# Optimization experiments

Hardware: AMD Instinct MI355X
Metric: run time of the kernel (lower is better)

The kernel has to match this reference:

```python
import jax, jax.numpy as jnp
import numpy as np

NEG_SLOPE = 0.01  # torch nn.LeakyReLU default
N_NODES = 100000
N_EDGES = 500000
IN_DIM, OUT_DIM, EF_DIM, EMB_DIM = 128, 128, 64, 256


def leaky_relu(x):
    return jnp.where(x >= 0, x, NEG_SLOPE * x)


def setup_inputs() -> dict:
    key = jax.random.key(0)
    ks = jax.random.split(key, 8)
    s = 0.05
    nf = jax.random.normal(ks[0], (N_NODES, IN_DIM), dtype=jnp.float32)
    ef = jax.random.normal(ks[1], (N_EDGES, EF_DIM), dtype=jnp.float32)
    src = jax.random.randint(ks[2], (N_EDGES,), 0, N_NODES, dtype=jnp.int32)
    dst = jax.random.randint(ks[3], (N_EDGES,), 0, N_NODES, dtype=jnp.int32)
    # Linear weights stored as (in, out); y = x @ W. No biases (bias=False).
    We1 = jax.random.normal(ks[4], (2 * IN_DIM + EF_DIM, EMB_DIM), dtype=jnp.float32) * s
    We2 = jax.random.normal(ks[5], (EMB_DIM, OUT_DIM), dtype=jnp.float32) * s
    Wn1 = jax.random.normal(ks[6], (IN_DIM + OUT_DIM, EMB_DIM), dtype=jnp.float32) * s
    Wn2 = jax.random.normal(ks[7], (EMB_DIM, OUT_DIM), dtype=jnp.float32) * s
    return {"nf": nf, "ef": ef, "src": src, "dst": dst,
            "We1": We1, "We2": We2, "Wn1": Wn1, "Wn2": Wn2}


def reference(nf, ef, src, dst, We1, We2, Wn1, Wn2):
    # Symmetrize: add reversed edges carrying the same edge features.
    src_full = jnp.concatenate([src, dst])            # [2E]
    dst_full = jnp.concatenate([dst, src])            # [2E]
    ef_full = jnp.concatenate([ef, ef], axis=0)       # [2E, ef_dim]

    # message_func: MLP over [src_nf | dst_nf | ef]
    edge_in = jnp.concatenate([nf[src_full], nf[dst_full], ef_full], axis=-1)  # [2E, 2*in+ef]
    msg = leaky_relu(edge_in @ We1) @ We2              # [2E, out]

    # reduce_func: sum messages per destination node (zeros for isolated nodes)
    red = jax.ops.segment_sum(msg, dst_full, num_segments=nf.shape[0])  # [N, out]

    # apply_node_func: MLP over [nf | red_msg]
    node_in = jnp.concatenate([nf, red], axis=-1)      # [N, in+out]
    out_nf = leaky_relu(node_in @ Wn1) @ Wn2           # [N, out]
    return out_nf
```

## Files before the change

kernel.cpp:

```cpp
#include <hip/hip_runtime.h>
#include <hip/hip_bf16.h>
#include <string.h>


using f32x4  = __attribute__((ext_vector_type(4))) float;
using bf16x8 = __attribute__((ext_vector_type(8))) short;

#define P128 132
#define P256 264
#define YROW 132

__device__ __forceinline__ float lrelu(float x) { return x >= 0.f ? x : 0.01f * x; }

__device__ __forceinline__ ushort f2bf(float f) {
    union { float f; unsigned u; } v; v.f = f;
    unsigned u = v.u;
    return (ushort)((u + 0x7fffu + ((u >> 16) & 1u)) >> 16);
}
__device__ __forceinline__ float bf2f(ushort u) {
    union { unsigned u; float f; } v; v.u = ((unsigned)u) << 16; return v.f;
}

__device__ __forceinline__ void atomic_pk_add_bf16(void* addr, unsigned val) {
    asm volatile("global_atomic_pk_add_bf16 %0, %1, off" : : "v"(addr), "v"(val) : "memory");
}

__global__ __launch_bounds__(256) void gemm_ab(
    const ushort* __restrict__ X,
    const ushort* __restrict__ Wt,
    ushort* __restrict__ out)
{
    __shared__ ushort Xs[128 * P128];
    const int tid  = threadIdx.x;
    const int lane = tid & 63;
    const int wv   = tid >> 6;
    const int wm   = wv >> 1, wn = wv & 1;
    const int row0 = blockIdx.x * 128;

    #pragma unroll
    for (int q = 0; q < 8; ++q) {
        int idx = q * 256 + tid;
        int r = idx >> 4, c = idx & 15;
        *reinterpret_cast<uint4*>(&Xs[r * P128 + c * 8]) =
            *reinterpret_cast<const uint4*>(X + (size_t)(row0 + r) * 128 + c * 8);
    }
    __syncthreads();

    const int g8 = (lane >> 4) * 8;
    for (int cb = 0; cb < 4; ++cb) {
        f32x4 acc[4][4] = {};
        #pragma unroll
        for (int ks = 0; ks < 4; ++ks) {
            bf16x8 af[4], bf[4];
            #pragma unroll
            for (int i = 0; i < 4; ++i) {
                int mrow = wm * 64 + i * 16 + (lane & 15);
                af[i] = *reinterpret_cast<const bf16x8*>(&Xs[mrow * P128 + ks * 32 + g8]);
                int nc = cb * 128 + wn * 64 + i * 16 + (lane & 15);
                bf[i] = *reinterpret_cast<const bf16x8*>(Wt + (size_t)nc * 128 + ks * 32 + g8);
            }
            #pragma unroll
            for (int i = 0; i < 4; ++i)
                #pragma unroll
                for (int j = 0; j < 4; ++j)
                    acc[i][j] = __builtin_amdgcn_mfma_f32_16x16x32_bf16(af[i], bf[j], acc[i][j], 0, 0, 0);
        }
        #pragma unroll
        for (int i = 0; i < 4; ++i) {
            int gr0 = row0 + wm * 64 + i * 16 + ((lane >> 4) << 2);
            #pragma unroll
            for (int j = 0; j < 4; ++j) {
                int gc = cb * 128 + wn * 64 + j * 16 + (lane & 15);
                #pragma unroll
                for (int r = 0; r < 4; ++r)
                    out[(size_t)(gr0 + r) * 512 + gc] = f2bf(acc[i][j][r]);
            }
        }
    }
}

__global__ __launch_bounds__(256) void edge_msg(
    const ushort* __restrict__ efb,
    const ushort* __restrict__ Wet,
    const ushort* __restrict__ We2t,
    const ushort* __restrict__ AB,
    const int* __restrict__ src, const int* __restrict__ dst,
    ushort* __restrict__ H,
    int E)
{
    __shared__ ushort Ms[64 * P256];
    __shared__ ushort Cs[32 * P256];
    __shared__ int own_s[64], oth_s[64];

    const int tid  = threadIdx.x;
    const int lane = tid & 63;
    const int wv   = tid >> 6;
    const int eb   = blockIdx.x * 32;
    const int g8   = (lane >> 4) * 8;

    if (tid < 32) {
        int e = eb + tid;
        int s_ = (e < E) ? src[e] : -1;
        int d_ = (e < E) ? dst[e] : -1;
        own_s[tid]      = d_;
        oth_s[tid]      = (s_ < 0) ? 0 : s_;
        own_s[32 + tid] = s_;
        oth_s[32 + tid] = (d_ < 0) ? 0 : d_;
    }

    f32x4 ac[2][4] = {};
    #pragma unroll
    for (int ks = 0; ks < 2; ++ks) {
        bf16x8 af[2], bf[4];
        #pragma unroll
        for (int i = 0; i < 2; ++i) {
            int er = i * 16 + (lane & 15);
            af[i] = *reinterpret_cast<const bf16x8*>(efb + (size_t)(eb + er) * 64 + ks * 32 + g8);
        }
        #pragma unroll
        for (int j = 0; j < 4; ++j) {
            int nc = wv * 64 + j * 16 + (lane & 15);
            bf[j] = *reinterpret_cast<const bf16x8*>(Wet + (size_t)nc * 64 + ks * 32 + g8);
        }
        #pragma unroll
        for (int i = 0; i < 2; ++i)
            #pragma unroll
            for (int j = 0; j < 4; ++j)
                ac[i][j] = __builtin_amdgcn_mfma_f32_16x16x32_bf16(af[i], bf[j], ac[i][j], 0, 0, 0);
    }
    #pragma unroll
    for (int i = 0; i < 2; ++i) {
        int er0 = i * 16 + ((lane >> 4) << 2);
        #pragma unroll
        for (int j = 0; j < 4; ++j) {
            int fc = wv * 64 + j * 16 + (lane & 15);
            #pragma unroll
            for (int r = 0; r < 4; ++r)
                Cs[(er0 + r) * P256 + fc] = f2bf(ac[i][j][r]);
        }
    }
    __syncthreads();

    #pragma unroll 4
    for (int p = 0; p < 16; ++p) {
        int m   = p * 4 + wv;
        int oth = oth_s[m];
        int own = own_s[m];
        int ownc = (own < 0) ? 0 : own;
        int rc  = m & 31;
        #pragma unroll
        for (int h = 0; h < 2; ++h) {
            int c = h * 128 + lane * 2;
            ushort2 av = *(const ushort2*)(AB + (size_t)oth  * 512 + c);
            ushort2 bv = *(const ushort2*)(AB + (size_t)ownc * 512 + 256 + c);
            ushort2 cv = *(const ushort2*)(&Cs[rc * P256 + c]);
            ushort2 mv;
            mv.x = f2bf(lrelu(bf2f(av.x) + bf2f(bv.x) + bf2f(cv.x)));
            mv.y = f2bf(lrelu(bf2f(av.y) + bf2f(bv.y) + bf2f(cv.y)));
            *(ushort2*)(&Ms[m * P256 + c]) = mv;
        }
    }
    __syncthreads();

    const int wm = wv >> 1, wn = wv & 1;
    f32x4 ay[2][4] = {};
    #pragma unroll
    for (int ks = 0; ks < 8; ++ks) {
        bf16x8 af[2], bf[4];
        #pragma unroll
        for (int i = 0; i < 2; ++i) {
            int mrow = wm * 32 + i * 16 + (lane & 15);
            af[i] = *reinterpret_cast<const bf16x8*>(&Ms[mrow * P256 + ks * 32 + g8]);
        }
        #pragma unroll
        for (int j = 0; j < 4; ++j) {
            int nc = wn * 64 + j * 16 + (lane & 15);
            bf[j] = *reinterpret_cast<const bf16x8*>(We2t + (size_t)nc * 256 + ks * 32 + g8);
        }
        #pragma unroll
        for (int i = 0; i < 2; ++i)
            #pragma unroll
            for (int j = 0; j < 4; ++j)
                ay[i][j] = __builtin_amdgcn_mfma_f32_16x16x32_bf16(af[i], bf[j], ay[i][j], 0, 0, 0);
    }
    ushort* Ys = Cs;
    #pragma unroll
    for (int i = 0; i < 2; ++i) {
        int yr0 = wm * 32 + i * 16 + ((lane >> 4) << 2);
        #pragma unroll
        for (int j = 0; j < 4; ++j) {
            int yc = wn * 64 + j * 16 + (lane & 15);
            #pragma unroll
            for (int r = 0; r < 4; ++r)
                Ys[(yr0 + r) * YROW + yc] = f2bf(ay[i][j][r]);
        }
    }
    __syncthreads();

    #pragma unroll 4
    for (int q = 0; q < 16; ++q) {
        int row  = wv * 16 + q;
        int node = own_s[row];
        if (node < 0) continue;
        ushort2 yv = *(const ushort2*)(&Ys[row * YROW + lane * 2]);
        unsigned uv; memcpy(&uv, &yv, 4);
        atomic_pk_add_bf16(H + (size_t)node * 128 + lane * 2, uv);
    }
}

__global__ __launch_bounds__(256) void mlp_fused(
    const ushort* __restrict__ H,
    const ushort* __restrict__ nfb,
    const ushort* __restrict__ Wn1t,
    const ushort* __restrict__ Wn2t,
    float* __restrict__ out, int Nreal)
{
    __shared__ ushort lds[128 * P256];
    ushort* Ns  = lds;
    ushort* Rs  = lds + 128 * P128;
    ushort* Hid = lds;

    const int tid  = threadIdx.x;
    const int lane = tid & 63;
    const int wv   = tid >> 6;
    const int wm   = wv >> 1, wn = wv & 1;
    const int row0 = blockIdx.x * 128;
    const int g8   = (lane >> 4) * 8;

    #pragma unroll
    for (int q = 0; q < 8; ++q) {
        int idx = q * 256 + tid;
        int r = idx >> 4, c = (idx & 15) * 8;
        *reinterpret_cast<uint4*>(&Ns[r * P128 + c]) =
            *reinterpret_cast<const uint4*>(nfb + (size_t)(row0 + r) * 128 + c);
        *reinterpret_cast<uint4*>(&Rs[r * P128 + c]) =
            *reinterpret_cast<const uint4*>(H + (size_t)(row0 + r) * 128 + c);
    }
    __syncthreads();

    f32x4 a2[2][4][4] = {};
    #pragma unroll
    for (int cb = 0; cb < 2; ++cb) {
        #pragma unroll
        for (int ks = 0; ks < 8; ++ks) {
            bf16x8 af[4], bf[4];
            #pragma unroll
            for (int i = 0; i < 4; ++i) {
                int mrow = wm * 64 + i * 16 + (lane & 15);
                af[i] = (ks < 4)
                    ? *reinterpret_cast<const bf16x8*>(&Ns[mrow * P128 + ks * 32 + g8])
                    : *reinterpret_cast<const bf16x8*>(&Rs[mrow * P128 + (ks - 4) * 32 + g8]);
                int nc = cb * 128 + wn * 64 + i * 16 + (lane & 15);
                bf[i] = *reinterpret_cast<const bf16x8*>(Wn1t + (size_t)nc * 256 + ks * 32 + g8);
            }
            #pragma unroll
            for (int i = 0; i < 4; ++i)
                #pragma unroll
                for (int j = 0; j < 4; ++j)
                    a2[cb][i][j] = __builtin_amdgcn_mfma_f32_16x16x32_bf16(af[i], bf[j], a2[cb][i][j], 0, 0, 0);
        }
    }
    __syncthreads();

    #pragma unroll
    for (int cb = 0; cb < 2; ++cb)
        #pragma unroll
        for (int i = 0; i < 4; ++i) {
            int er0 = wm * 64 + i * 16 + ((lane >> 4) << 2);
            #pragma unroll
            for (int j = 0; j < 4; ++j) {
                int fc = cb * 128 + wn * 64 + j * 16 + (lane & 15);
                #pragma unroll
                for (int r = 0; r < 4; ++r)
                    Hid[(er0 + r) * P256 + fc] = f2bf(lrelu(a2[cb][i][j][r]));
            }
        }
    __syncthreads();

    f32x4 a3[4][4] = {};
    #pragma unroll
    for (int ks = 0; ks < 8; ++ks) {
        bf16x8 af[4], bf[4];
        #pragma unroll
        for (int i = 0; i < 4; ++i) {
            int mrow = wm * 64 + i * 16 + (lane & 15);
            af[i] = *reinterpret_cast<const bf16x8*>(&Hid[mrow * P256 + ks * 32 + g8]);
            int nc = wn * 64 + i * 16 + (lane & 15);
            bf[i] = *reinterpret_cast<const bf16x8*>(Wn2t + (size_t)nc * 256 + ks * 32 + g8);
        }
        #pragma unroll
        for (int i = 0; i < 4; ++i)
            #pragma unroll
            for (int j = 0; j < 4; ++j)
                a3[i][j] = __builtin_amdgcn_mfma_f32_16x16x32_bf16(af[i], bf[j], a3[i][j], 0, 0, 0);
    }
    #pragma unroll
    for (int i = 0; i < 4; ++i) {
        int gr0 = row0 + wm * 64 + i * 16 + ((lane >> 4) << 2);
        #pragma unroll
        for (int j = 0; j < 4; ++j) {
            int gc = wn * 64 + j * 16 + (lane & 15);
            #pragma unroll
            for (int r = 0; r < 4; ++r) {
                int gr = gr0 + r;
                if (gr < Nreal) out[(size_t)gr * 128 + gc] = a3[i][j][r];
            }
        }
    }
}

__global__ __launch_bounds__(256) void cvt_pad(
    const float* __restrict__ x, ushort* __restrict__ y, size_t n_real, size_t n_pad)
{
    size_t i = ((size_t)blockIdx.x * 256 + threadIdx.x) * 4;
    if (i >= n_pad) return;
    ushort4 o;
    if (i < n_real) {
        float4 v = *(const float4*)(x + i);
        o.x = f2bf(v.x); o.y = f2bf(v.y); o.z = f2bf(v.z); o.w = f2bf(v.w);
    } else { o.x = 0; o.y = 0; o.z = 0; o.w = 0; }
    *(ushort4*)(y + i) = o;
}

__global__ __launch_bounds__(256) void wcvt(
    const float* __restrict__ We1, const float* __restrict__ We2,
    const float* __restrict__ Wn1, const float* __restrict__ Wn2,
    ushort* __restrict__ Wabt, ushort* __restrict__ Wet, ushort* __restrict__ We2t,
    ushort* __restrict__ Wn1t, ushort* __restrict__ Wn2t)
{
    int idx = blockIdx.x * 256 + threadIdx.x;
    switch (blockIdx.y) {
    case 0: if (idx < 256*128) { int n = idx >> 7, k = idx & 127; Wabt[idx]            = f2bf(We1[k * 256 + n]); } break;
    case 1: if (idx < 256*128) { int n = idx >> 7, k = idx & 127; Wabt[32768 + idx]    = f2bf(We1[(128 + k) * 256 + n]); } break;
    case 2: if (idx < 256*64)  { int n = idx >> 6, k = idx & 63;  Wet[idx]             = f2bf(We1[(256 + k) * 256 + n]); } break;
    case 3: if (idx < 128*256) { int n = idx >> 8, k = idx & 255; We2t[idx]            = f2bf(We2[k * 128 + n]); } break;
    case 4: if (idx < 256*256) { int n = idx >> 8, k = idx & 255; Wn1t[idx]            = f2bf(Wn1[k * 256 + n]); } break;
    case 5: if (idx < 128*256) { int n = idx >> 8, k = idx & 255; Wn2t[idx]            = f2bf(Wn2[k * 128 + n]); } break;
    }
}

extern "C" void kernel_launch(void* const* d_in, const int* in_sizes, int n_in,
                              void* d_out, int out_size, void* d_ws, size_t ws_size,
                              hipStream_t stream) {
    const float* nf  = (const float*)d_in[0];
    const float* ef  = (const float*)d_in[1];
    const int*   src = (const int*)d_in[2];
    const int*   dst = (const int*)d_in[3];
    const float* We1 = (const float*)d_in[4];
    const float* We2 = (const float*)d_in[5];
    const float* Wn1 = (const float*)d_in[6];
    const float* Wn2 = (const float*)d_in[7];
    float* out = (float*)d_out;

    const int  N  = in_sizes[0] / 128;
    const int  E  = in_sizes[2];
    const int  Np = (N + 127) & ~127;
    const long Ep = ((long)E + 127) & ~127L;

    char* p = (char*)d_ws;
    auto alloc = [&](size_t bytes) { char* r = p; p += (bytes + 255) & ~(size_t)255; return r; };
    ushort* AB   = (ushort*)alloc((size_t)Np * 512 * 2);
    ushort* H    = (ushort*)alloc((size_t)Np * 128 * 2);
    ushort* nfb  = (ushort*)alloc((size_t)Np * 128 * 2);
    ushort* efb  = (ushort*)alloc((size_t)Ep * 64 * 2);
    ushort* Wabt = (ushort*)alloc(65536 * 2);
    ushort* Wet  = (ushort*)alloc(16384 * 2);
    ushort* We2t = (ushort*)alloc(32768 * 2);
    ushort* Wn1t = (ushort*)alloc(65536 * 2);
    ushort* Wn2t = (ushort*)alloc(32768 * 2);

    dim3 blk(256);

    wcvt<<<dim3(256, 6), blk, 0, stream>>>(We1, We2, Wn1, Wn2, Wabt, Wet, We2t, Wn1t, Wn2t);
    cvt_pad<<<dim3((unsigned)((size_t)Np * 128 / 1024)), blk, 0, stream>>>(nf, nfb, (size_t)N * 128, (size_t)Np * 128);
    cvt_pad<<<dim3((unsigned)((size_t)Ep * 64 / 1024)), blk, 0, stream>>>(ef, efb, (size_t)E * 64, (size_t)Ep * 64);

    gemm_ab<<<dim3(Np / 128), blk, 0, stream>>>(nfb, Wabt, AB);

    hipMemsetAsync(H, 0, (size_t)Np * 128 * 2, stream);

    edge_msg<<<dim3((unsigned)(Ep / 32)), blk, 0, stream>>>(
        efb, Wet, We2t, AB, src, dst, H, E);

    mlp_fused<<<dim3(Np / 128), blk, 0, stream>>>(H, nfb, Wn1t, Wn2t, out, N);
}
```

Before: 771.5 us.

## Sort directed edges by destination and pre-reduce messages before atomic adds

Adds a counting sort (count, single-block scan, scatter) that groups the 2E directed edge records by owning destination node. The edge kernel now processes 64 sorted records per block, gathers edge features by index, prefetches gathered AB rows in registers across phases, and sums consecutive messages for the same node locally before one bf16 atomic per run. The aim is fewer global atomics and better locality on the destination side. In exchange it adds several launches, a serial single-block scan over 100k nodes, atomic scatter ordering, and an indirect edge-feature gather.

```diff
diff --git a/kernel.cpp b/kernel.cpp
--- a/kernel.cpp
+++ b/kernel.cpp
@@ -9,6 +9,7 @@
 #define P128 132
 #define P256 264
 #define YROW 132
+#define VPB  64
 
 __device__ __forceinline__ float lrelu(float x) { return x >= 0.f ? x : 0.01f * x; }
 
@@ -79,84 +80,169 @@
     }
 }
 
-__global__ __launch_bounds__(256) void edge_msg(
+__global__ __launch_bounds__(256) void ebin_count(
+    const int* __restrict__ src, const int* __restrict__ dst,
+    int* __restrict__ cnt, int E)
+{
+    int i = blockIdx.x * 256 + threadIdx.x;
+    if (i >= E) return;
+    atomicAdd(&cnt[dst[i]], 1);
+    atomicAdd(&cnt[src[i]], 1);
+}
+
+__global__ __launch_bounds__(256) void escan(
+    const int* __restrict__ cnt, int* __restrict__ cur, int n)
+{
+    __shared__ int ps[256];
+    const int t = threadIdx.x;
+    const int per = (n + 255) / 256;
+    int s = 0;
+    for (int i = 0; i < per; ++i) { int idx = t * per + i; if (idx < n) s += cnt[idx]; }
+    ps[t] = s;
+    __syncthreads();
+    for (int off = 1; off < 256; off <<= 1) {
+        int u = (t >= off) ? ps[t - off] : 0;
+        __syncthreads();
+        ps[t] += u;
+        __syncthreads();
+    }
+    int run = ps[t] - s;
+    for (int i = 0; i < per; ++i) {
+        int idx = t * per + i;
+        if (idx < n) { cur[idx] = run; run += cnt[idx]; }
+    }
+}
+
+__global__ __launch_bounds__(256) void escatter(
+    const int* __restrict__ src, const int* __restrict__ dst,
+    int* __restrict__ cur, int4* __restrict__ vrec, int E)
+{
+    int i = blockIdx.x * 256 + threadIdx.x;
+    if (i >= E) return;
+    int s_ = src[i], d_ = dst[i];
+    int p1 = atomicAdd(&cur[d_], 1);
+    vrec[p1] = make_int4(d_, s_, i, 0);
+    int p2 = atomicAdd(&cur[s_], 1);
+    vrec[p2] = make_int4(s_, d_, i, 0);
+}
+
+__global__ __launch_bounds__(256) void edge_sorted(
     const ushort* __restrict__ efb,
     const ushort* __restrict__ Wet,
     const ushort* __restrict__ We2t,
     const ushort* __restrict__ AB,
-    const int* __restrict__ src, const int* __restrict__ dst,
+    const int4* __restrict__ vrec,
     ushort* __restrict__ H,
-    int E)
-{
-    __shared__ ushort Ms[64 * P256];
-    __shared__ ushort Cs[32 * P256];
-    __shared__ int own_s[64], oth_s[64];
+    int NV)
+{
+    __shared__ ushort Ms[VPB * P256];
+    __shared__ ushort efs[VPB * 72];
+    __shared__ int so[VPB], st_[VPB], se[VPB];
 
     const int tid  = threadIdx.x;
     const int lane = tid & 63;
     const int wv   = tid >> 6;
-    const int eb   = blockIdx.x * 32;
     const int g8   = (lane >> 4) * 8;
-
-    if (tid < 32) {
-        int e = eb + tid;
-        int s_ = (e < E) ? src[e] : -1;
-        int d_ = (e < E) ? dst[e] : -1;
-        own_s[tid]      = d_;
-        oth_s[tid]      = (s_ < 0) ? 0 : s_;
-        own_s[32 + tid] = s_;
-        oth_s[32 + tid] = (d_ < 0) ? 0 : d_;
-    }
-
-    f32x4 ac[2][4] = {};
-    #pragma unroll
-    for (int ks = 0; ks < 2; ++ks) {
-        bf16x8 af[2], bf[4];
-        #pragma unroll
-        for (int i = 0; i < 2; ++i) {
-            int er = i * 16 + (lane & 15);
-            af[i] = *reinterpret_cast<const bf16x8*>(efb + (size_t)(eb + er) * 64 + ks * 32 + g8);
-        }
-        #pragma unroll
-        for (int j = 0; j < 4; ++j) {
-            int nc = wv * 64 + j * 16 + (lane & 15);
-            bf[j] = *reinterpret_cast<const bf16x8*>(Wet + (size_t)nc * 64 + ks * 32 + g8);
-        }
-        #pragma unroll
-        for (int i = 0; i < 2; ++i)
-            #pragma unroll
-            for (int j = 0; j < 4; ++j)
-                ac[i][j] = __builtin_amdgcn_mfma_f32_16x16x32_bf16(af[i], bf[j], ac[i][j], 0, 0, 0);
-    }
-    #pragma unroll
-    for (int i = 0; i < 2; ++i) {
-        int er0 = i * 16 + ((lane >> 4) << 2);
-        #pragma unroll
-        for (int j = 0; j < 4; ++j) {
-            int fc = wv * 64 + j * 16 + (lane & 15);
-            #pragma unroll
-            for (int r = 0; r < 4; ++r)
-                Cs[(er0 + r) * P256 + fc] = f2bf(ac[i][j][r]);
-        }
-    }
-    __syncthreads();
-
-    #pragma unroll 4
-    for (int p = 0; p < 16; ++p) {
-        int m   = p * 4 + wv;
-        int oth = oth_s[m];
-        int own = own_s[m];
-        int ownc = (own < 0) ? 0 : own;
-        int rc  = m & 31;
+    const int v0   = blockIdx.x * VPB;
+
+    if (tid < VPB) {
+        int v = v0 + tid;
+        if (v < NV) { int4 r = vrec[v]; so[tid] = r.x; st_[tid] = r.y; se[tid] = r.z; }
+        else        { so[tid] = -1; st_[tid] = 0; se[tid] = 0; }
+    }
+    __syncthreads();
+
+    ushort2 av0[8][2], bv0[8][2];
+    #pragma unroll
+    for (int u = 0; u < 8; ++u) {
+        int m = wv * 16 + u;
+        int oth = st_[m];
+        int own = so[m] < 0 ? 0 : so[m];
+        #pragma unroll
+        for (int h = 0; h < 2; ++h) {
+            av0[u][h] = *(const ushort2*)(AB + (size_t)oth * 512 + h * 128 + lane * 2);
+            bv0[u][h] = *(const ushort2*)(AB + (size_t)own * 512 + 256 + h * 128 + lane * 2);
+        }
+    }
+
+    #pragma unroll
+    for (int q = 0; q < 2; ++q) {
+        int row = q * 32 + (tid >> 3);
+        *reinterpret_cast<uint4*>(&efs[row * 72 + (tid & 7) * 8]) =
+            *reinterpret_cast<const uint4*>(efb + (size_t)se[row] * 64 + (tid & 7) * 8);
+    }
+    __syncthreads();
+
+    {
+        f32x4 ac[4][4] = {};
+        #pragma unroll
+        for (int ks = 0; ks < 2; ++ks) {
+            bf16x8 af[4], bf[4];
+            #pragma unroll
+            for (int i = 0; i < 4; ++i) {
+                int er = i * 16 + (lane & 15);
+                af[i] = *reinterpret_cast<const bf16x8*>(&efs[er * 72 + ks * 32 + g8]);
+            }
+            #pragma unroll
+            for (int j = 0; j < 4; ++j) {
+                int nc = wv * 64 + j * 16 + (lane & 15);
+                bf[j] = *reinterpret_cast<const bf16x8*>(Wet + (size_t)nc * 64 + ks * 32 + g8);
+            }
+            #pragma unroll
+            for (int i = 0; i < 4; ++i)
+                #pragma unroll
+                for (int j = 0; j < 4; ++j)
+                    ac[i][j] = __builtin_amdgcn_mfma_f32_16x16x32_bf16(af[i], bf[j], ac[i][j], 0, 0, 0);
+        }
+        #pragma unroll
+        for (int i = 0; i < 4; ++i) {
+            int er0 = i * 16 + ((lane >> 4) << 2);
+            #pragma unroll
+            for (int j = 0; j < 4; ++j) {
+                int fc = wv * 64 + j * 16 + (lane & 15);
+                #pragma unroll
+                for (int r = 0; r < 4; ++r)
+                    Ms[(er0 + r) * P256 + fc] = f2bf(ac[i][j][r]);
+            }
+        }
+    }
+    __syncthreads();
+
+    ushort2 av1[8][2], bv1[8][2];
+    #pragma unroll
+    for (int u = 0; u < 8; ++u) {
+        int m = wv * 16 + 8 + u;
+        int oth = st_[m];
+        int own = so[m] < 0 ? 0 : so[m];
+        #pragma unroll
+        for (int h = 0; h < 2; ++h) {
+            av1[u][h] = *(const ushort2*)(AB + (size_t)oth * 512 + h * 128 + lane * 2);
+            bv1[u][h] = *(const ushort2*)(AB + (size_t)own * 512 + 256 + h * 128 + lane * 2);
+        }
+    }
+    #pragma unroll
+    for (int u = 0; u < 8; ++u) {
+        int m = wv * 16 + u;
         #pragma unroll
         for (int h = 0; h < 2; ++h) {
             int c = h * 128 + lane * 2;
-            ushort2 av = *(const ushort2*)(AB + (size_t)oth  * 512 + c);
-            ushort2 bv = *(const ushort2*)(AB + (size_t)ownc * 512 + 256 + c);
-            ushort2 cv = *(const ushort2*)(&Cs[rc * P256 + c]);
+            ushort2 cv = *(const ushort2*)(&Ms[m * P256 + c]);
             ushort2 mv;
-            mv.x = f2bf(lrelu(bf2f(av.x) + bf2f(bv.x) + bf2f(cv.x)));
-            mv.y = f2bf(lrelu(bf2f(av.y) + bf2f(bv.y) + bf2f(cv.y)));
+            mv.x = f2bf(lrelu(bf2f(av0[u][h].x) + bf2f(bv0[u][h].x) + bf2f(cv.x)));
+            mv.y = f2bf(lrelu(bf2f(av0[u][h].y) + bf2f(bv0[u][h].y) + bf2f(cv.y)));
+            *(ushort2*)(&Ms[m * P256 + c]) = mv;
+        }
+    }
+    #pragma unroll
+    for (int u = 0; u < 8; ++u) {
+        int m = wv * 16 + 8 + u;
+        #pragma unroll
+        for (int h = 0; h < 2; ++h) {
+            int c = h * 128 + lane * 2;
+            ushort2 cv = *(const ushort2*)(&Ms[m * P256 + c]);
+            ushort2 mv;
+            mv.x = f2bf(lrelu(bf2f(av1[u][h].x) + bf2f(bv1[u][h].x) + bf2f(cv.x)));
+            mv.y = f2bf(lrelu(bf2f(av1[u][h].y) + bf2f(bv1[u][h].y) + bf2f(cv.y)));
             *(ushort2*)(&Ms[m * P256 + c]) = mv;
         }
     }
@@ -183,7 +269,9 @@
             for (int j = 0; j < 4; ++j)
                 ay[i][j] = __builtin_amdgcn_mfma_f32_16x16x32_bf16(af[i], bf[j], ay[i][j], 0, 0, 0);
     }
-    ushort* Ys = Cs;
+    __syncthreads();
+
+    ushort* Ys = Ms;
     #pragma unroll
     for (int i = 0; i < 2; ++i) {
         int yr0 = wm * 32 + i * 16 + ((lane >> 4) << 2);
@@ -197,14 +285,29 @@
     }
     __syncthreads();
 
-    #pragma unroll 4
-    for (int q = 0; q < 16; ++q) {
-        int row  = wv * 16 + q;
-        int node = own_s[row];
-        if (node < 0) continue;
-        ushort2 yv = *(const ushort2*)(&Ys[row * YROW + lane * 2]);
-        unsigned uv; memcpy(&uv, &yv, 4);
-        atomic_pk_add_bf16(H + (size_t)node * 128 + lane * 2, uv);
+    {
+        float a0 = 0.f, a1 = 0.f;
+        int cur = so[wv * 16];
+        #pragma unroll 4
+        for (int q = 0; q < 16; ++q) {
+            int row = wv * 16 + q;
+            int own = so[row];
+            ushort2 yv = *(const ushort2*)(&Ys[row * YROW + lane * 2]);
+            float y0 = bf2f(yv.x), y1 = bf2f(yv.y);
+            if (own != cur) {
+                if (cur >= 0) {
+                    ushort2 o; o.x = f2bf(a0); o.y = f2bf(a1);
+                    unsigned uv; memcpy(&uv, &o, 4);
+                    atomic_pk_add_bf16(H + (size_t)cur * 128 + lane * 2, uv);
+                }
+                cur = own; a0 = y0; a1 = y1;
+            } else { a0 += y0; a1 += y1; }
+        }
+        if (cur >= 0) {
+            ushort2 o; o.x = f2bf(a0); o.y = f2bf(a1);
+            unsigned uv; memcpy(&uv, &o, 4);
+            atomic_pk_add_bf16(H + (size_t)cur * 128 + lane * 2, uv);
+        }
     }
 }
 
@@ -356,6 +459,7 @@
     const int  E  = in_sizes[2];
     const int  Np = (N + 127) & ~127;
     const long Ep = ((long)E + 127) & ~127L;
+    const int  NV = 2 * E;
 
     char* p = (char*)d_ws;
     auto alloc = [&](size_t bytes) { char* r = p; p += (bytes + 255) & ~(size_t)255; return r; };
@@ -368,19 +472,28 @@
     ushort* We2t = (ushort*)alloc(32768 * 2);
     ushort* Wn1t = (ushort*)alloc(65536 * 2);
     ushort* Wn2t = (ushort*)alloc(32768 * 2);
+    int*    cnt  = (int*)alloc((size_t)N * 4);
+    int*    curp = (int*)alloc((size_t)N * 4);
+    int4*   vrec = (int4*)alloc((size_t)NV * 16);
 
     dim3 blk(256);
+    const unsigned egrid = (unsigned)((E + 255) / 256);
 
     wcvt<<<dim3(256, 6), blk, 0, stream>>>(We1, We2, Wn1, Wn2, Wabt, Wet, We2t, Wn1t, Wn2t);
     cvt_pad<<<dim3((unsigned)((size_t)Np * 128 / 1024)), blk, 0, stream>>>(nf, nfb, (size_t)N * 128, (size_t)Np * 128);
     cvt_pad<<<dim3((unsigned)((size_t)Ep * 64 / 1024)), blk, 0, stream>>>(ef, efb, (size_t)E * 64, (size_t)Ep * 64);
 
+    hipMemsetAsync(cnt, 0, (size_t)N * 4, stream);
+    ebin_count<<<dim3(egrid), blk, 0, stream>>>(src, dst, cnt, E);
+    escan<<<dim3(1), blk, 0, stream>>>(cnt, curp, N);
+    escatter<<<dim3(egrid), blk, 0, stream>>>(src, dst, curp, vrec, E);
+
     gemm_ab<<<dim3(Np / 128), blk, 0, stream>>>(nfb, Wabt, AB);
 
     hipMemsetAsync(H, 0, (size_t)Np * 128 * 2, stream);
 
-    edge_msg<<<dim3((unsigned)(Ep / 32)), blk, 0, stream>>>(
-        efb, Wet, We2t, AB, src, dst, H, E);
+    edge_sorted<<<dim3((unsigned)((NV + VPB - 1) / VPB)), blk, 0, stream>>>(
+        efb, Wet, We2t, AB, vrec, H, NV);
 
     mlp_fused<<<dim3(Np / 128), blk, 0, stream>>>(H, nfb, Wn1t, Wn2t, out, N);
 }
```

After: 1.123 ms. 1.46x slower.
